# Optimization experiments

Hardware: AMD Instinct MI355X
Metric: run time of the kernel (lower is better)

## Reference

```python
import jax, jax.numpy as jnp
import numpy as np

N_STATE = 1024
N_HEAD = 16
D_K = N_STATE // N_HEAD  # 64


def setup_inputs() -> dict:
    key = jax.random.key(0)
    ks = jax.random.split(key, 12)
    B, S = 2, 2048
    s = 1.0 / np.sqrt(N_STATE)
    inp = {
        "q": jax.random.normal(ks[0], (B, S, N_STATE), jnp.float32),
        "k": jax.random.normal(ks[1], (B, S, N_STATE), jnp.float32),
        "v": jax.random.normal(ks[2], (B, S, N_STATE), jnp.float32),
        # Linear weights in torch layout [out_features, in_features]
        "Wq": jax.random.normal(ks[3], (N_STATE, N_STATE), jnp.float32) * s,
        "bq": jax.random.normal(ks[4], (N_STATE,), jnp.float32) * s,
        "Wk": jax.random.normal(ks[5], (N_STATE, N_STATE), jnp.float32) * s,
        "bk": jax.random.normal(ks[6], (N_STATE,), jnp.float32) * s,
        "Wv": jax.random.normal(ks[7], (N_STATE, N_STATE), jnp.float32) * s,
        "bv": jax.random.normal(ks[8], (N_STATE,), jnp.float32) * s,
        "Wo": jax.random.normal(ks[9], (N_STATE, N_STATE), jnp.float32) * s,
        "bo": jax.random.normal(ks[10], (N_STATE,), jnp.float32) * s,
    }
    return inp


def reference(q, k, v, Wq, bq, Wk, bk, Wv, bv, Wo, bo):
    B = q.shape[0]
    # projections (torch Linear: x @ W.T + b), split heads -> [B, H, S, d]
    def proj(x, W, b):
        y = jnp.einsum('bsi,oi->bso', x, W) + b
        return y.reshape(B, -1, N_HEAD, D_K).transpose(0, 2, 1, 3)
    qh = proj(q, Wq, bq)
    kh = proj(k, Wk, bk)
    vh = proj(v, Wv, bv)
    # scaled dot-product attention, full [B,H,Sq,Sk] scores as in original
    scores = jnp.einsum('bhqd,bhkd->bhqk', qh, kh) / np.sqrt(D_K).astype(np.float32)
    attn = jax.nn.softmax(scores, axis=-1)
    out = jnp.einsum('bhqk,bhkd->bhqd', attn, vh)
    out = out.transpose(0, 2, 1, 3).reshape(B, -1, N_HEAD * D_K)
    return jnp.einsum('bsi,oi->bso', out, Wo) + bo
```

## Files before the change

### kernel.cpp

```cpp
#include <hip/hip_runtime.h>
#include <hip/hip_bf16.h>
#include <stdint.h>

typedef __attribute__((ext_vector_type(8))) short short8;
typedef __attribute__((ext_vector_type(4))) float f32x4;
typedef __attribute__((ext_vector_type(4))) uint32_t u32x4;

#if __has_builtin(__builtin_amdgcn_exp2f)
#define EXP2(x) __builtin_amdgcn_exp2f(x)
#else
#define EXP2(x) exp2f(x)
#endif

__device__ __forceinline__ short f2bf(float f){
  uint32_t u = __builtin_bit_cast(uint32_t, f);
  return (short)((u + 0x8000u) >> 16);
}
__device__ __forceinline__ uint32_t pk2(float lo, float hi){
  __hip_bfloat162 h = __float22bfloat162_rn(make_float2(lo, hi));
  uint32_t u; __builtin_memcpy(&u, &h, 4); return u;
}
__device__ __forceinline__ void gload16(const void* g, void* l){
  __builtin_amdgcn_global_load_lds((const __attribute__((address_space(1))) void*)g,
                                   (__attribute__((address_space(3))) void*)l, 16, 0, 0);
}

__global__ __launch_bounds__(512) void cvt_all(
    const float* __restrict__ q, const float* __restrict__ k, const float* __restrict__ v,
    const float* __restrict__ wq, const float* __restrict__ wk, const float* __restrict__ wv,
    const float* __restrict__ wo, short* __restrict__ dst){
  const size_t SQ = 4096ull*1024ull, NW = 1024ull*1024ull;
  size_t e = (size_t)(blockIdx.x*512u + threadIdx.x)*8ull;
  const float* src; size_t rel;
  if (e < 3*SQ){ size_t which = e / SQ; src = which==0?q:(which==1?k:v); rel = e - which*SQ; }
  else { size_t e2 = e - 3*SQ; size_t which = e2 / NW;
         src = which==0?wq:(which==1?wk:(which==2?wv:wo)); rel = e2 - which*NW; }
  float4 a = *(const float4*)(src + rel);
  float4 b = *(const float4*)(src + rel + 4);
  u32x4 r = { pk2(a.x,a.y), pk2(a.z,a.w), pk2(b.x,b.y), pk2(b.z,b.w) };
  *(u32x4*)(dst + e) = r;
}

template<int MODE>
__device__ __forceinline__ void gemm_body(const short* __restrict__ A, const short* __restrict__ Bw,
    const float* __restrict__ bias, void* __restrict__ Cout, float scale, int m0, int n0){
  const int K = 1024;
  __shared__ short Al[128*64];
  __shared__ short Bl[128*64];
  int tid = threadIdx.x;
  int w = tid >> 6, lane = tid & 63, lr = lane & 15, lg = lane >> 4;
  int wr = w >> 2, wc = w & 3;
  f32x4 acc[4][2] = {};
  int row0 = tid >> 3;
  int qc0  = (tid & 7) ^ (row0 & 7);
  const short* Ag = A  + (size_t)(m0 + row0)*K + qc0*8;
  const short* Bg = Bw + (size_t)(n0 + row0)*K + qc0*8;
  char* Alb = (char*)Al + tid*16;
  char* Blb = (char*)Bl + tid*16;
  int ra[4], rb[2];
#pragma unroll
  for (int mi=0; mi<4; ++mi) ra[mi] = wr*64 + mi*16 + lr;
#pragma unroll
  for (int ni=0; ni<2; ++ni) rb[ni] = wc*32 + ni*16 + lr;
  for (int k0 = 0; k0 < K; k0 += 64){
    gload16(Ag + k0,                Alb);
    gload16(Ag + k0 + 64*(size_t)K, Alb + 8192);
    gload16(Bg + k0,                Blb);
    gload16(Bg + k0 + 64*(size_t)K, Blb + 8192);
    __syncthreads();
#pragma unroll
    for (int kk=0; kk<2; ++kk){
      short8 av[4], bv[2];
#pragma unroll
      for (int mi=0; mi<4; ++mi)
        av[mi] = *(const short8*)((char*)Al + ra[mi]*128 + (((kk*4 + lg) ^ (ra[mi] & 7)) << 4));
#pragma unroll
      for (int ni=0; ni<2; ++ni)
        bv[ni] = *(const short8*)((char*)Bl + rb[ni]*128 + (((kk*4 + lg) ^ (rb[ni] & 7)) << 4));
#pragma unroll
      for (int mi=0; mi<4; ++mi)
#pragma unroll
        for (int ni=0; ni<2; ++ni){
          if (MODE == 2)
            acc[mi][ni] = __builtin_amdgcn_mfma_f32_16x16x32_bf16(bv[ni], av[mi], acc[mi][ni], 0, 0, 0);
          else
            acc[mi][ni] = __builtin_amdgcn_mfma_f32_16x16x32_bf16(av[mi], bv[ni], acc[mi][ni], 0, 0, 0);
        }
    }
    __syncthreads();
  }
#pragma unroll
  for (int ni=0; ni<2; ++ni){
#pragma unroll
    for (int mi=0; mi<4; ++mi){
      if (MODE == 2){
        int srow = m0 + wr*64 + mi*16 + lr;
        int b = srow >> 11, s = srow & 2047;
#pragma unroll
        for (int i2=0; i2<4; ++i2){
          int dcol = n0 + wc*32 + ni*16 + lg*4 + i2;
          int h = dcol >> 6, d = dcol & 63;
          float val = acc[mi][ni][i2] + bias[dcol];
          ((short*)Cout)[(((size_t)(b*16 + h))*64 + d)*2048 + s] = f2bf(val);
        }
      } else {
        int col = n0 + wc*32 + ni*16 + lr;
        float bb = bias[col];
#pragma unroll
        for (int i2=0; i2<4; ++i2){
          int row = m0 + wr*64 + mi*16 + lg*4 + i2;
          float val = (acc[mi][ni][i2] + bb) * scale;
          if (MODE == 0){
            int b = row >> 11, s = row & 2047, h = col >> 6, d = col & 63;
            ((short*)Cout)[(((size_t)(b*16 + h))*2048 + s)*64 + d] = f2bf(val);
          } else {
            ((float*)Cout)[(size_t)row*1024 + col] = val;
          }
        }
      }
    }
  }
}

__global__ __launch_bounds__(512) void gemm_qkv(
    const short* __restrict__ qb, const short* __restrict__ kb, const short* __restrict__ vb,
    const short* __restrict__ Wqb, const short* __restrict__ Wkb, const short* __restrict__ Wvb,
    const float* __restrict__ bq, const float* __restrict__ bk, const float* __restrict__ bv,
    short* __restrict__ Qh, short* __restrict__ Kh, short* __restrict__ VhT, float qscale){
  int f = blockIdx.y*gridDim.x + blockIdx.x;
  int L = (f & 7)*96 + (f >> 3);
  int z = L >> 8, r = L & 255;
  int m0 = (r >> 3)*128, n0 = (r & 7)*128;
  const short* A  = z==0 ? qb  : (z==1 ? kb  : vb);
  const short* Bw = z==0 ? Wqb : (z==1 ? Wkb : Wvb);
  const float* bi = z==0 ? bq  : (z==1 ? bk  : bv);
  short* C        = z==0 ? Qh  : (z==1 ? Kh  : VhT);
  if (z == 2) gemm_body<2>(A, Bw, bi, (void*)C, 1.0f, m0, n0);
  else        gemm_body<0>(A, Bw, bi, (void*)C, z==0 ? qscale : 1.0f, m0, n0);
}

__global__ __launch_bounds__(512) void gemm_out(const short* __restrict__ A, const short* __restrict__ Bw,
    const float* __restrict__ bias, float* __restrict__ Cout){
  int f = blockIdx.y*gridDim.x + blockIdx.x;
  int L = (f & 7)*32 + (f >> 3);
  int m0 = (L >> 3)*128, n0 = (L & 7)*128;
  gemm_body<1>(A, Bw, bias, (void*)Cout, 1.0f, m0, n0);
}

__global__ __launch_bounds__(512) void attn_fwd(const short* __restrict__ Qh, const short* __restrict__ Kh,
    const short* __restrict__ VhT, short* __restrict__ AO){
  const int S = 2048;
  int i = blockIdx.y*gridDim.x + blockIdx.x;
  int L = (i & 7)*64 + (i >> 3);
  int bh = L >> 4, qt = L & 15;
  __shared__ short Kl[4][4096];
  __shared__ short Vl[4][4096];
  int tid = threadIdx.x, w = tid >> 6, lane = tid & 63, lr = lane & 15, lg = lane >> 4;
  const short* Qb = Qh  + (size_t)bh*S*64;
  const short* Kb = Kh  + (size_t)bh*S*64;
  const short* Vb = VhT + (size_t)bh*64*2048;
  int q0 = qt*128 + w*16;
  short8 aq[2];
#pragma unroll
  for (int h=0; h<2; ++h)
    aq[h] = *(const short8*)&Qb[(size_t)(q0 + lr)*64 + h*32 + lg*8];
  f32x4 o[4] = {};
  f32x4 o1 = {};
  short8 ones;
#pragma unroll
  for (int j=0; j<8; ++j) ones[j] = (short)0x3F80;
  int koff = tid*16;
  int kr = tid >> 3, kc = tid & 7;
  int ksw = (kr & 3) | (((kr >> 3) & 1) << 2);
  int ksrc = kr*64 + ((kc ^ ksw) << 3);
  int vsrc = kr*2048 + ((kc ^ (kr & 7)) << 3);
  int Rbase = 8*(lr >> 2) + (lr & 3);
  int sR = (lr & 3) | (((lr >> 2) & 1) << 2);
  int slot0 = (lg ^ sR) << 3, slot1 = ((lg + 4) ^ sR) << 3;
  int vx = lr & 7;
  gload16(Kb + ksrc,        (char*)&Kl[0][0] + koff);
  gload16(Vb + vsrc,        (char*)&Vl[0][0] + koff);
  gload16(Kb + 4096 + ksrc, (char*)&Kl[1][0] + koff);
  gload16(Vb + vsrc + 64,   (char*)&Vl[1][0] + koff);
  asm volatile("s_waitcnt vmcnt(2) lgkmcnt(0)" ::: "memory");
  __builtin_amdgcn_sched_barrier(0);
  __builtin_amdgcn_s_barrier();

  for (int t = 0; t < 32; ++t){
    int buf = t & 3;
    if (t + 2 < 32){
      int nb = (t + 2) & 3;
      gload16(Kb + (size_t)(t + 2)*4096 + ksrc, (char*)&Kl[nb][0] + koff);
      gload16(Vb + vsrc + (t + 2)*64,           (char*)&Vl[nb][0] + koff);
    }
    const short* Kbuf = &Kl[buf][0];
    uint32_t Wp[2][2][2];
    __builtin_amdgcn_s_setprio(1);
#pragma unroll
    for (int nf=0; nf<4; ++nf){
      int R = Rbase + (nf & 1)*4 + (nf >> 1)*32;
      short8 ak0 = *(const short8*)&Kbuf[R*64 + slot0];
      short8 ak1 = *(const short8*)&Kbuf[R*64 + slot1];
      f32x4 z = {};
      z = __builtin_amdgcn_mfma_f32_16x16x32_bf16(ak0, aq[0], z, 0, 0, 0);
      z = __builtin_amdgcn_mfma_f32_16x16x32_bf16(ak1, aq[1], z, 0, 0, 0);
      float p0 = EXP2(z[0]), p1 = EXP2(z[1]);
      float p2 = EXP2(z[2]), p3 = EXP2(z[3]);
      Wp[nf >> 1][nf & 1][0] = pk2(p0, p1);
      Wp[nf >> 1][nf & 1][1] = pk2(p2, p3);
    }
    __builtin_amdgcn_s_setprio(0);
    short8 pa[2];
#pragma unroll
    for (int c=0; c<2; ++c){
      union { uint32_t u[4]; short8 s; } tt;
      tt.u[0] = Wp[c][0][0]; tt.u[1] = Wp[c][0][1];
      tt.u[2] = Wp[c][1][0]; tt.u[3] = Wp[c][1][1];
      pa[c] = tt.s;
    }
    const short* Vbuf = &Vl[buf][0];
    __builtin_amdgcn_s_setprio(1);
#pragma unroll
    for (int df=0; df<4; ++df){
      int rowv = (df*16 + lr)*64;
      short8 vb0 = *(const short8*)&Vbuf[rowv + ((lg ^ vx) << 3)];
      short8 vb1 = *(const short8*)&Vbuf[rowv + (((4 + lg) ^ vx) << 3)];
      o[df] = __builtin_amdgcn_mfma_f32_16x16x32_bf16(pa[0], vb0, o[df], 0, 0, 0);
      o[df] = __builtin_amdgcn_mfma_f32_16x16x32_bf16(pa[1], vb1, o[df], 0, 0, 0);
    }
    o1 = __builtin_amdgcn_mfma_f32_16x16x32_bf16(pa[0], ones, o1, 0, 0, 0);
    o1 = __builtin_amdgcn_mfma_f32_16x16x32_bf16(pa[1], ones, o1, 0, 0, 0);
    __builtin_amdgcn_s_setprio(0);
    if (t + 1 < 32){
      if (t < 30) asm volatile("s_waitcnt vmcnt(2)" ::: "memory");
      else        asm volatile("s_waitcnt vmcnt(0)" ::: "memory");
      __builtin_amdgcn_sched_barrier(0);
      __builtin_amdgcn_s_barrier();
    }
  }
  int b = bh >> 4, hh = bh & 15;
  float rinv[4];
#pragma unroll
  for (int i2=0; i2<4; ++i2) rinv[i2] = 1.0f / o1[i2];
#pragma unroll
  for (int df=0; df<4; ++df)
#pragma unroll
    for (int i2=0; i2<4; ++i2){
      int row = q0 + lg*4 + i2;
      int col = df*16 + lr;
      AO[((size_t)(b*2048 + row))*1024 + hh*64 + col] = f2bf(o[df][i2] * rinv[i2]);
    }
}

extern "C" void kernel_launch(void* const* d_in, const int* in_sizes, int n_in,
                              void* d_out, int out_size, void* d_ws, size_t ws_size,
                              hipStream_t stream){
  const float* q  = (const float*)d_in[0];
  const float* k  = (const float*)d_in[1];
  const float* v  = (const float*)d_in[2];
  const float* Wq = (const float*)d_in[3];
  const float* bq = (const float*)d_in[4];
  const float* Wk = (const float*)d_in[5];
  const float* bk = (const float*)d_in[6];
  const float* Wv = (const float*)d_in[7];
  const float* bv = (const float*)d_in[8];
  const float* Wo = (const float*)d_in[9];
  const float* bo = (const float*)d_in[10];

  const size_t SQ = 4096ull*1024ull, NW = 1024ull*1024ull;
  short* ws  = (short*)d_ws;
  short* qb  = ws;
  short* kb  = ws + SQ;
  short* vb  = ws + 2*SQ;
  short* Wqb = ws + 3*SQ;
  short* Wkb = Wqb + NW;
  short* Wvb = Wkb + NW;
  short* Wob = Wvb + NW;
  short* Qh  = Wob + NW;
  short* Kh  = Qh + SQ;
  short* VhT = Kh + SQ;
  short* AO  = qb;

  const float Csc = 0.18033688011112042f;

  cvt_all<<<4096, 512, 0, stream>>>(q, k, v, Wq, Wk, Wv, Wo, ws);
  gemm_qkv<<<dim3(16, 48), 512, 0, stream>>>(qb, kb, vb, Wqb, Wkb, Wvb, bq, bk, bv, Qh, Kh, VhT, Csc);
  attn_fwd<<<dim3(16, 32), 512, 0, stream>>>(Qh, Kh, VhT, AO);
  gemm_out<<<dim3(16, 16), 512, 0, stream>>>(AO, Wob, bo, (float*)d_out);
}
```

Before: 115.9 us.

## Process two KV tiles per barrier and use cheap bf16 packing

```diff
diff --git a/kernel.cpp b/kernel.cpp
--- a/kernel.cpp
+++ b/kernel.cpp
@@ -1,5 +1,4 @@
 #include <hip/hip_runtime.h>
-#include <hip/hip_bf16.h>
 #include <stdint.h>
 
 typedef __attribute__((ext_vector_type(8))) short short8;
@@ -17,8 +16,13 @@
   return (short)((u + 0x8000u) >> 16);
 }
 __device__ __forceinline__ uint32_t pk2(float lo, float hi){
-  __hip_bfloat162 h = __float22bfloat162_rn(make_float2(lo, hi));
-  uint32_t u; __builtin_memcpy(&u, &h, 4); return u;
+  uint32_t a = __builtin_bit_cast(uint32_t, lo) + 0x8000u;
+  uint32_t b = __builtin_bit_cast(uint32_t, hi) + 0x8000u;
+#if __has_builtin(__builtin_amdgcn_perm)
+  return __builtin_amdgcn_perm(b, a, 0x07060302u);
+#else
+  return (b & 0xFFFF0000u) | (a >> 16);
+#endif
 }
 __device__ __forceinline__ void gload16(const void* g, void* l){
   __builtin_amdgcn_global_load_lds((const __attribute__((address_space(1))) void*)g,
@@ -178,64 +182,70 @@
   int sR = (lr & 3) | (((lr >> 2) & 1) << 2);
   int slot0 = (lg ^ sR) << 3, slot1 = ((lg + 4) ^ sR) << 3;
   int vx = lr & 7;
-  gload16(Kb + ksrc,        (char*)&Kl[0][0] + koff);
-  gload16(Vb + vsrc,        (char*)&Vl[0][0] + koff);
-  gload16(Kb + 4096 + ksrc, (char*)&Kl[1][0] + koff);
-  gload16(Vb + vsrc + 64,   (char*)&Vl[1][0] + koff);
-  asm volatile("s_waitcnt vmcnt(2) lgkmcnt(0)" ::: "memory");
+#pragma unroll
+  for (int t=0; t<4; ++t){
+    gload16(Kb + (size_t)t*4096 + ksrc, (char*)&Kl[t][0] + koff);
+    gload16(Vb + vsrc + t*64,           (char*)&Vl[t][0] + koff);
+  }
+  asm volatile("s_waitcnt vmcnt(4)" ::: "memory");
   __builtin_amdgcn_sched_barrier(0);
   __builtin_amdgcn_s_barrier();
 
-  for (int t = 0; t < 32; ++t){
-    int buf = t & 3;
-    if (t + 2 < 32){
-      int nb = (t + 2) & 3;
-      gload16(Kb + (size_t)(t + 2)*4096 + ksrc, (char*)&Kl[nb][0] + koff);
-      gload16(Vb + vsrc + (t + 2)*64,           (char*)&Vl[nb][0] + koff);
-    }
-    const short* Kbuf = &Kl[buf][0];
-    uint32_t Wp[2][2][2];
+  for (int p = 0; p < 16; ++p){
+    short8 pa[2][2];
     __builtin_amdgcn_s_setprio(1);
 #pragma unroll
-    for (int nf=0; nf<4; ++nf){
-      int R = Rbase + (nf & 1)*4 + (nf >> 1)*32;
-      short8 ak0 = *(const short8*)&Kbuf[R*64 + slot0];
-      short8 ak1 = *(const short8*)&Kbuf[R*64 + slot1];
-      f32x4 z = {};
-      z = __builtin_amdgcn_mfma_f32_16x16x32_bf16(ak0, aq[0], z, 0, 0, 0);
-      z = __builtin_amdgcn_mfma_f32_16x16x32_bf16(ak1, aq[1], z, 0, 0, 0);
-      float p0 = EXP2(z[0]), p1 = EXP2(z[1]);
-      float p2 = EXP2(z[2]), p3 = EXP2(z[3]);
-      Wp[nf >> 1][nf & 1][0] = pk2(p0, p1);
-      Wp[nf >> 1][nf & 1][1] = pk2(p2, p3);
+    for (int u = 0; u < 2; ++u){
+      const short* Kbuf = &Kl[(2*p + u) & 3][0];
+      uint32_t Wp[2][2][2];
+#pragma unroll
+      for (int nf=0; nf<4; ++nf){
+        int R = Rbase + (nf & 1)*4 + (nf >> 1)*32;
+        short8 ak0 = *(const short8*)&Kbuf[R*64 + slot0];
+        short8 ak1 = *(const short8*)&Kbuf[R*64 + slot1];
+        f32x4 z = {};
+        z = __builtin_amdgcn_mfma_f32_16x16x32_bf16(ak0, aq[0], z, 0, 0, 0);
+        z = __builtin_amdgcn_mfma_f32_16x16x32_bf16(ak1, aq[1], z, 0, 0, 0);
+        float p0 = EXP2(z[0]), p1 = EXP2(z[1]);
+        float p2 = EXP2(z[2]), p3 = EXP2(z[3]);
+        Wp[nf >> 1][nf & 1][0] = pk2(p0, p1);
+        Wp[nf >> 1][nf & 1][1] = pk2(p2, p3);
+      }
+#pragma unroll
+      for (int c=0; c<2; ++c){
+        union { uint32_t u4[4]; short8 s; } tt;
+        tt.u4[0] = Wp[c][0][0]; tt.u4[1] = Wp[c][0][1];
+        tt.u4[2] = Wp[c][1][0]; tt.u4[3] = Wp[c][1][1];
+        pa[u][c] = tt.s;
+      }
+    }
+#pragma unroll
+    for (int u = 0; u < 2; ++u){
+      const short* Vbuf = &Vl[(2*p + u) & 3][0];
+#pragma unroll
+      for (int df=0; df<4; ++df){
+        int rowv = (df*16 + lr)*64;
+        short8 vb0 = *(const short8*)&Vbuf[rowv + ((lg ^ vx) << 3)];
+        short8 vb1 = *(const short8*)&Vbuf[rowv + (((4 + lg) ^ vx) << 3)];
+        o[df] = __builtin_amdgcn_mfma_f32_16x16x32_bf16(pa[u][0], vb0, o[df], 0, 0, 0);
+        o[df] = __builtin_amdgcn_mfma_f32_16x16x32_bf16(pa[u][1], vb1, o[df], 0, 0, 0);
+      }
+      o1 = __builtin_amdgcn_mfma_f32_16x16x32_bf16(pa[u][0], ones, o1, 0, 0, 0);
+      o1 = __builtin_amdgcn_mfma_f32_16x16x32_bf16(pa[u][1], ones, o1, 0, 0, 0);
     }
     __builtin_amdgcn_s_setprio(0);
-    short8 pa[2];
-#pragma unroll
-    for (int c=0; c<2; ++c){
-      union { uint32_t u[4]; short8 s; } tt;
-      tt.u[0] = Wp[c][0][0]; tt.u[1] = Wp[c][0][1];
-      tt.u[2] = Wp[c][1][0]; tt.u[3] = Wp[c][1][1];
-      pa[c] = tt.s;
-    }
-    const short* Vbuf = &Vl[buf][0];
-    __builtin_amdgcn_s_setprio(1);
-#pragma unroll
-    for (int df=0; df<4; ++df){
-      int rowv = (df*16 + lr)*64;
-      short8 vb0 = *(const short8*)&Vbuf[rowv + ((lg ^ vx) << 3)];
-      short8 vb1 = *(const short8*)&Vbuf[rowv + (((4 + lg) ^ vx) << 3)];
-      o[df] = __builtin_amdgcn_mfma_f32_16x16x32_bf16(pa[0], vb0, o[df], 0, 0, 0);
-      o[df] = __builtin_amdgcn_mfma_f32_16x16x32_bf16(pa[1], vb1, o[df], 0, 0, 0);
-    }
-    o1 = __builtin_amdgcn_mfma_f32_16x16x32_bf16(pa[0], ones, o1, 0, 0, 0);
-    o1 = __builtin_amdgcn_mfma_f32_16x16x32_bf16(pa[1], ones, o1, 0, 0, 0);
-    __builtin_amdgcn_s_setprio(0);
-    if (t + 1 < 32){
-      if (t < 30) asm volatile("s_waitcnt vmcnt(2)" ::: "memory");
-      else        asm volatile("s_waitcnt vmcnt(0)" ::: "memory");
+    if (p < 15){
+      asm volatile("s_waitcnt vmcnt(0)" ::: "memory");
       __builtin_amdgcn_sched_barrier(0);
       __builtin_amdgcn_s_barrier();
+      if (p < 14){
+#pragma unroll
+        for (int u = 0; u < 2; ++u){
+          int t = 2*p + 4 + u, nb = t & 3;
+          gload16(Kb + (size_t)t*4096 + ksrc, (char*)&Kl[nb][0] + koff);
+          gload16(Vb + vsrc + t*64,           (char*)&Vl[nb][0] + koff);
+        }
+      }
     }
   }
   int b = bh >> 4, hh = bh & 15;
```

Result: no change. 115.0 us (-0.8%).
